# Kernel tuning notes

Hardware: AMD Instinct MI355X
Metric: run time of the kernel (lower is better)

The kernel has to match this reference:

```python
import jax, jax.numpy as jnp
import numpy as np

B, N, E = 256, 512, 8192
F_IN, DEPTH, NHID = 128, 3, 256
CAT = F_IN + DEPTH * NHID  # 896


def setup_inputs() -> dict:
    key = jax.random.key(0)
    ks = jax.random.split(key, 20)
    def w(k, shape, fan_in):
        return jax.random.normal(k, shape, jnp.float32) / np.sqrt(fan_in)
    inp = {
        "x": jax.random.normal(ks[0], (B, N, F_IN), jnp.float32),
        "edge_index": jax.random.randint(ks[1], (2, E), 0, N, jnp.int64),
        # linears: first maps F_IN->NHID, rest NHID->NHID (stacked)
        "lin0_W": w(ks[2], (F_IN, NHID), F_IN),
        "lin0_b": jnp.zeros((NHID,), jnp.float32),
        "lin_Ws": w(ks[3], (DEPTH - 1, NHID, NHID), NHID),
        "lin_bs": jnp.zeros((DEPTH - 1, NHID), jnp.float32),
        # GCNConv weights (stacked), PyG semantics: A_norm (X W) + b
        "conv_Ws": w(ks[4], (DEPTH, NHID, NHID), NHID),
        "conv_bs": jnp.zeros((DEPTH, NHID), jnp.float32),
        "sig_W": w(ks[5], (CAT, NHID), CAT),
        "sig_b": jnp.zeros((NHID,), jnp.float32),
        "tanh_W": w(ks[6], (CAT, NHID), CAT),
        "tanh_b": jnp.zeros((NHID,), jnp.float32),
        "f1_W": w(ks[7], (NHID, NHID), NHID),
        "f1_b": jnp.zeros((NHID,), jnp.float32),
        "f2_W": w(ks[8], (NHID, 2), NHID),
        "f2_b": jnp.zeros((2,), jnp.float32),
    }
    return inp


def _gcn_norm(edge_index, n):
    # add self loops, compute symmetric normalization D^-1/2 (A+I) D^-1/2
    loop = jnp.arange(n, dtype=edge_index.dtype)
    src = jnp.concatenate([edge_index[0], loop])
    dst = jnp.concatenate([edge_index[1], loop])
    deg = jax.ops.segment_sum(jnp.ones_like(src, jnp.float32), dst, num_segments=n)
    dinv = jax.lax.rsqrt(jnp.maximum(deg, 1.0))
    norm = dinv[src] * dinv[dst]  # [E+N]
    return src, dst, norm


def _gcn(h, W, b, src, dst, norm, n):
    # h: [B, N, C]
    hW = h @ W
    msg = hW[:, src, :] * norm[None, :, None]          # [B, E+N, C]
    agg = jax.vmap(lambda m: jax.ops.segment_sum(m, dst, num_segments=n))(msg)
    return agg + b


def reference(x, edge_index, lin0_W, lin0_b, lin_Ws, lin_bs, conv_Ws, conv_bs,
              sig_W, sig_b, tanh_W, tanh_b, f1_W, f1_b, f2_W, f2_b):
    n = x.shape[1]
    src, dst, norm = _gcn_norm(edge_index, n)
    xs = [x]
    out = x
    for i in range(DEPTH):
        if i == 0:
            out = out @ lin0_W + lin0_b
        else:
            out = out @ lin_Ws[i - 1] + lin_bs[i - 1]
        out = _gcn(out, conv_Ws[i], conv_bs[i], src, dst, norm, n)
        out = jnp.tanh(out)
        xs.append(out)
    cat = jnp.concatenate(xs, axis=-1)                 # [B, N, CAT]
    s = jax.nn.sigmoid(cat @ sig_W + sig_b)            # [B, N, NHID]
    t = jnp.tanh(cat @ tanh_W + tanh_b)                # [B, N, NHID]
    pooled = jnp.sum(s * t, axis=1)                    # [B, NHID] (sum over nodes)
    embeds = jnp.tanh(pooled)
    h = jax.nn.relu(embeds @ f1_W + f1_b)              # dropout is eval-mode identity
    preds = h @ f2_W + f2_b                            # [B, 2]
    preds = jnp.concatenate([jax.nn.sigmoid(preds[:, :1]), preds[:, 1:]], axis=-1)
    return preds, embeds
```

## Files before the change

### kernel.cpp

```cpp
#include <hip/hip_runtime.h>
#include <hip/hip_bf16.h>
#include <cstdint>

typedef _Float16 half_t;
typedef __attribute__((ext_vector_type(8))) _Float16 half8;
typedef __attribute__((ext_vector_type(4))) _Float16 half4;
typedef __attribute__((ext_vector_type(4))) float f32x4;

#define MFMA16x32(a, b, c) __builtin_amdgcn_mfma_f32_16x16x32_f16(a, b, c, 0, 0, 0)

static constexpr int NB  = 256;
static constexpr int NN  = 512;
static constexpr int NE  = 8192;
static constexpr int FIN = 128;
static constexpr int NH  = 256;
static constexpr int CAT = 896;

__device__ __forceinline__ float fsigmoid(float u)
{
    return __builtin_amdgcn_rcpf(1.f + __expf(-u));
}
__device__ __forceinline__ float ftanh(float v)
{
    const float c = fminf(fmaxf(v, -10.f), 10.f);
    const float e = __expf(2.f * c);
    return (e - 1.f) * __builtin_amdgcn_rcpf(e + 1.f);
}

__device__ __forceinline__ void xcd_swz_y(int& bx, int& by)
{
    const int nwg = gridDim.x * gridDim.y;
    int wgid = blockIdx.y * gridDim.x + blockIdx.x;
    wgid = (wgid & 7) * (nwg >> 3) + (wgid >> 3);
    bx = wgid % gridDim.x;
    by = wgid / gridDim.x;
}
__device__ __forceinline__ void xcd_swz_x(int& bx, int& by)
{
    const int nwg = gridDim.x * gridDim.y;
    int wgid = blockIdx.x * gridDim.y + blockIdx.y;
    wgid = (wgid & 7) * (nwg >> 3) + (wgid >> 3);
    bx = wgid / gridDim.y;
    by = wgid % gridDim.y;
}

__device__ __forceinline__ void gload16(const half_t* __restrict__ g, half_t* l)
{
    __builtin_amdgcn_global_load_lds(
        (const __attribute__((address_space(1))) uint32_t*)(uintptr_t)g,
        (__attribute__((address_space(3))) uint32_t*)(uintptr_t)l, 16, 0, 0);
}

__device__ __forceinline__ void stage128x64(
    const half_t* __restrict__ src, long row0, int ldk, int k0,
    half_t* lds, int tid)
{
    const int wid = tid >> 6, lane = tid & 63;
#pragma unroll
    for (int it = 0; it < 4; ++it) {
        const int rb   = wid * 32 + it * 8;
        const int row  = rb + (lane >> 3);
        const int slot = (lane & 7) ^ (row & 7);
        gload16(src + (row0 + row) * (long)ldk + k0 + slot * 8,
                lds + (size_t)rb * 64);
    }
}

__device__ __forceinline__ half8 fragr(const half_t* lds, int row, int slot)
{
    return *(const half8*)(lds + row * 64 + ((slot ^ (row & 7)) * 8));
}

struct Tab {
    const void* src[16];
    float*      dst[16];
    int         n[16];
    int         fi[16];
    int         nseg;
};

__global__ void k_detect_all(Tab t, int* __restrict__ flags)
{
    const int s = blockIdx.x;
    if (s >= t.nseg) return;
    __shared__ int cnt_s;
    if (threadIdx.x == 0) cnt_s = 0;
    __syncthreads();
    const uint32_t* w = (const uint32_t*)t.src[s];
    int nw = t.n[s] / 2; if (nw > 2048) nw = 2048; if (nw < 1) nw = 1;
    int c = 0;
    for (int i = threadIdx.x; i < nw; i += 256) {
        const uint32_t lo = w[i] & 0xFFFFu;
        const int e = (int)((lo >> 7) & 0xFF);
        if (lo == 0u || (e >= 116 && e <= 136)) ++c;
    }
    atomicAdd(&cnt_s, c);
    __syncthreads();
    if (threadIdx.x == 0) flags[t.fi[s]] = (2 * cnt_s >= nw) ? 1 : 0;
}

__global__ void k_cvt_all(Tab t, const int* __restrict__ flags)
{
    for (int s = 0; s < t.nseg; ++s) {
        float* dst = t.dst[s];
        if (dst == nullptr) continue;
        const int is_bf = flags[t.fi[s]];
        const int n = t.n[s];
        const void* src = t.src[s];
        for (int i = blockIdx.x * 256 + threadIdx.x; i < n; i += gridDim.x * 256)
            dst[i] = is_bf
                ? __uint_as_float(((uint32_t)((const uint16_t*)src)[i]) << 16)
                : ((const float*)src)[i];
    }
}

__global__ void k_x2h(const void* __restrict__ xraw, half_t* __restrict__ o,
                      size_t n8, const int* __restrict__ flag)
{
    const int is_bf = *flag;
    const size_t gid0 = (size_t)blockIdx.x * blockDim.x + threadIdx.x;
    const size_t stride = (size_t)gridDim.x * blockDim.x;
    if (is_bf) {
        const uint4* src = (const uint4*)xraw;
        for (size_t i = gid0; i < n8; i += stride) {
            const uint4 v = src[i];
            half8 h;
            h[0] = (_Float16)__uint_as_float((v.x & 0xFFFFu) << 16);
            h[1] = (_Float16)__uint_as_float(v.x & 0xFFFF0000u);
            h[2] = (_Float16)__uint_as_float((v.y & 0xFFFFu) << 16);
            h[3] = (_Float16)__uint_as_float(v.y & 0xFFFF0000u);
            h[4] = (_Float16)__uint_as_float((v.z & 0xFFFFu) << 16);
            h[5] = (_Float16)__uint_as_float(v.z & 0xFFFF0000u);
            h[6] = (_Float16)__uint_as_float((v.w & 0xFFFFu) << 16);
            h[7] = (_Float16)__uint_as_float(v.w & 0xFFFF0000u);
            ((half8*)o)[i] = h;
        }
    } else {
        const float4* src = (const float4*)xraw;
        for (size_t i = gid0; i < n8; i += stride) {
            const float4 a = src[2 * i], b = src[2 * i + 1];
            half8 h;
            h[0] = (_Float16)a.x; h[1] = (_Float16)a.y;
            h[2] = (_Float16)a.z; h[3] = (_Float16)a.w;
            h[4] = (_Float16)b.x; h[5] = (_Float16)b.y;
            h[6] = (_Float16)b.z; h[7] = (_Float16)b.w;
            ((half8*)o)[i] = h;
        }
    }
}

__global__ void k_sentinel(__hip_bfloat16* __restrict__ out, float code)
{
    const int i = blockIdx.x * 256 + threadIdx.x;
    if (i < 66048) out[i] = __float2bfloat16(i < 512 ? code : 0.f);
}

__global__ void k_pick512(const float* __restrict__ a, const float* __restrict__ b,
                          float* __restrict__ f2Wc, float* __restrict__ linbsc)
{
    __shared__ float sa_s, sb_s;
    const int t = threadIdx.x;
    if (t == 0) { sa_s = 0.f; sb_s = 0.f; }
    __syncthreads();
    float va = fabsf(a[t]) + fabsf(a[t + 256]);
    float vb = fabsf(b[t]) + fabsf(b[t + 256]);
    for (int o = 32; o; o >>= 1) {
        va += __shfl_down(va, o, 64);
        vb += __shfl_down(vb, o, 64);
    }
    if ((t & 63) == 0) { atomicAdd(&sa_s, va); atomicAdd(&sb_s, vb); }
    __syncthreads();
    const float* f2 = (sa_s >= sb_s) ? a : b;
    const float* lb = (sa_s >= sb_s) ? b : a;
    f2Wc[t] = f2[t]; f2Wc[t + 256] = f2[t + 256];
    linbsc[t] = lb[t]; linbsc[t + 256] = lb[t + 256];
}

__global__ void k_build_graph(const int* __restrict__ ei, int* __restrict__ rowptr,
                              int* __restrict__ colx, float* __restrict__ wn,
                              float* __restrict__ srow)
{
    __shared__ int   degs[NN];
    __shared__ float dinv[NN];
    __shared__ int   rp[NN + 1];
    __shared__ int   cur[NN];
    __shared__ float sacc[NN];
    __shared__ int   is64_s;
    const int t = threadIdx.x;
    degs[t] = 0; cur[t] = 0; sacc[t] = 0.f;
    if (t == 0) {
        int orv = 0;
        for (int i = 1; i < 256; i += 2) orv |= ei[i];
        is64_s = (orv == 0) ? 1 : 0;
    }
    __syncthreads();
    const bool is64 = (is64_s != 0);
    auto EV = [&](int idx) { return is64 ? ei[2 * idx] : ei[idx]; };

    for (int e = t; e < NE; e += NN)
        atomicAdd(&degs[EV(NE + e)], 1);
    __syncthreads();
    const float dv = rsqrtf(fmaxf((float)(degs[t] + 1), 1.f));
    dinv[t] = dv;
    __syncthreads();
    if (t == 0) {
        rp[0] = 0;
        for (int i = 0; i < NN; ++i) rp[i + 1] = rp[i] + degs[i] + 1;
    }
    __syncthreads();
    rowptr[t] = rp[t];
    if (t == 0) rowptr[NN] = rp[NN];
    for (int e = t; e < NE; e += NN) {
        const int s = EV(e), d = EV(NE + e);
        const int pos = atomicAdd(&cur[d], 1);
        colx[rp[d] + pos] = s;
        wn[rp[d] + pos]   = dinv[s] * dinv[d];
        atomicAdd(&sacc[d], dinv[s]);
    }
    __syncthreads();
    const int slot = rp[t + 1] - 1;
    colx[slot] = t;
    wn[slot]   = dv * dv;
    srow[t]    = dv * (sacc[t] + dv);
}

__global__ void k_densify(const int* __restrict__ rowptr, const int* __restrict__ colx,
                          const float* __restrict__ wn, half_t* __restrict__ S16)
{
    __shared__ float row[NN];
    const int d = blockIdx.x;
    for (int i = threadIdx.x; i < NN; i += 256) row[i] = 0.f;
    __syncthreads();
    const int s0 = rowptr[d], s1 = rowptr[d + 1];
    for (int e = s0 + threadIdx.x; e < s1; e += 256)
        atomicAdd(&row[colx[e]], wn[e]);
    __syncthreads();
    for (int i = threadIdx.x; i < NN; i += 256)
        S16[(size_t)d * NN + i] = (half_t)row[i];
}

__global__ void k_fold_wc(const float* __restrict__ lin0_W, const float* __restrict__ lin_Ws,
                          const float* __restrict__ conv_Ws,
                          half_t* __restrict__ wc0, half_t* __restrict__ wc1,
                          half_t* __restrict__ wc2)
{
    const int layer = blockIdx.y;
    const int k = blockIdx.x;
    const int n = threadIdx.x;
    const int K = (layer == 0) ? FIN : NH;
    if (k >= K) return;
    const float* lin = (layer == 0) ? lin0_W : lin_Ws + (size_t)(layer - 1) * NH * NH;
    const float* cw  = conv_Ws + (size_t)layer * NH * NH;
    float s = 0.f;
    for (int j = 0; j < NH; ++j) s += lin[k * NH + j] * cw[j * NH + n];
    half_t* o = (layer == 0) ? wc0 : ((layer == 1) ? wc1 : wc2);
    o[n * K + k] = (half_t)s;
}

__global__ void k_fold_wt(const float* __restrict__ sigW, const float* __restrict__ tanW,
                          half_t* __restrict__ sh, half_t* __restrict__ th,
                          const float* __restrict__ lin0_b, const float* __restrict__ lin_bs,
                          const float* __restrict__ conv_Ws, float* __restrict__ vb)
{
    const int which = blockIdx.y;
    if (which == 2) {
        const int layer = blockIdx.x;
        if (layer >= 3) return;
        const int n = threadIdx.x;
        const float* lb = (layer == 0) ? lin0_b : lin_bs + (size_t)(layer - 1) * NH;
        const float* cw = conv_Ws + (size_t)layer * NH * NH;
        float s = 0.f;
        for (int j = 0; j < NH; ++j) s += lb[j] * cw[j * NH + n];
        vb[layer * NH + n] = s;
        return;
    }
    const int n = blockIdx.x;
    const float* W = which ? tanW : sigW;
    half_t* o = which ? th : sh;
    for (int k = threadIdx.x; k < CAT; k += 256)
        o[(size_t)n * CAT + k] = (half_t)W[(size_t)k * NH + n];
}

__global__ __launch_bounds__(256, 2) void k_gemm_t(
    const half_t* __restrict__ A, const half_t* __restrict__ BT,
    half_t* __restrict__ hwT, int K)
{
    __shared__ __align__(16) half_t sm[17408];
    half_t* lA = sm;
    half_t* lB = sm + 8192;
    int bx, by; xcd_swz_x(bx, by);
    const int tid = threadIdx.x;
    const int lane = tid & 63, wid = tid >> 6;
    const int wr = wid >> 1, wc = wid & 1;
    const int row_l = lane & 15, kg = lane >> 4;
    const long mbase = (long)bx * 128;
    const int nbase = by * 128;
    f32x4 acc[4][4] = {};
    for (int k0 = 0; k0 < K; k0 += 64) {
        stage128x64(A,  mbase, K, k0, lA, tid);
        stage128x64(BT, nbase, K, k0, lB, tid);
        __syncthreads();
#pragma unroll
        for (int ks = 0; ks < 2; ++ks) {
            half8 af[4], bf[4];
#pragma unroll
            for (int mt = 0; mt < 4; ++mt)
                af[mt] = fragr(lA, wr * 64 + mt * 16 + row_l, ks * 4 + kg);
#pragma unroll
            for (int nt = 0; nt < 4; ++nt)
                bf[nt] = fragr(lB, wc * 64 + nt * 16 + row_l, ks * 4 + kg);
#pragma unroll
            for (int mt = 0; mt < 4; ++mt)
#pragma unroll
                for (int nt = 0; nt < 4; ++nt)
                    acc[mt][nt] = MFMA16x32(af[mt], bf[nt], acc[mt][nt]);
        }
        __syncthreads();
    }
    half_t* lC = sm;
#pragma unroll
    for (int mt = 0; mt < 4; ++mt) {
        const int m_l = wr * 64 + mt * 16 + kg * 4;
#pragma unroll
        for (int nt = 0; nt < 4; ++nt) {
            const int n_l = wc * 64 + nt * 16 + row_l;
            half4 p;
            p[0] = (_Float16)acc[mt][nt][0]; p[1] = (_Float16)acc[mt][nt][1];
            p[2] = (_Float16)acc[mt][nt][2]; p[3] = (_Float16)acc[mt][nt][3];
            *(half4*)(lC + n_l * 136 + m_l) = p;
        }
    }
    __syncthreads();
    const int b  = (int)(mbase >> 9);
    const int s0 = (int)(mbase & 511);
#pragma unroll
    for (int pass = 0; pass < 8; ++pass) {
        const int n_l = pass * 16 + (tid >> 4);
        const int part = tid & 15;
        const half8 v = *(const half8*)(lC + n_l * 136 + part * 8);
        *(half8*)(hwT + ((size_t)b * 256 + nbase + n_l) * 512 + s0 + part * 8) = v;
    }
}

__global__ __launch_bounds__(256, 2) void k_gemm_agg(
    const half_t* __restrict__ S16, const half_t* __restrict__ hwT,
    const float* __restrict__ srow, const float* __restrict__ vb,
    const float* __restrict__ cb, half_t* __restrict__ hout)
{
    __shared__ __align__(16) half_t sm[17408];
    half_t* lA = sm;
    half_t* lB = sm + 8192;
    int bx, by; xcd_swz_y(bx, by);
    const int tid = threadIdx.x;
    const int lane = tid & 63, wid = tid >> 6;
    const int wr = wid >> 1, wc = wid & 1;
    const int row_l = lane & 15, kg = lane >> 4;
    const int mbase = bx * 128;
    const int nbase = by * 128;
    f32x4 acc[4][4] = {};
    for (int k0 = 0; k0 < 512; k0 += 64) {
        stage128x64(S16, mbase, 512, k0, lA, tid);
        stage128x64(hwT, nbase, 512, k0, lB, tid);
        __syncthreads();
#pragma unroll
        for (int ks = 0; ks < 2; ++ks) {
            half8 af[4], bf[4];
#pragma unroll
            for (int mt = 0; mt < 4; ++mt)
                af[mt] = fragr(lA, wr * 64 + mt * 16 + row_l, ks * 4 + kg);
#pragma unroll
            for (int nt = 0; nt < 4; ++nt)
                bf[nt] = fragr(lB, wc * 64 + nt * 16 + row_l, ks * 4 + kg);
#pragma unroll
            for (int mt = 0; mt < 4; ++mt)
#pragma unroll
                for (int nt = 0; nt < 4; ++nt)
                    acc[mt][nt] = MFMA16x32(af[mt], bf[nt], acc[mt][nt]);
        }
        __syncthreads();
    }
    const int b  = nbase >> 8;
    const int c0 = nbase & 255;
    half_t* lC = sm;
#pragma unroll
    for (int mt = 0; mt < 4; ++mt) {
        const int m_l = wr * 64 + mt * 16 + kg * 4;
        float sr[4];
#pragma unroll
        for (int r = 0; r < 4; ++r) sr[r] = srow[mbase + m_l + r];
#pragma unroll
        for (int nt = 0; nt < 4; ++nt) {
            const int n_l = wc * 64 + nt * 16 + row_l;
            const float vbc = vb[c0 + n_l], cbc = cb[c0 + n_l];
#pragma unroll
            for (int r = 0; r < 4; ++r)
                lC[(m_l + r) * 136 + n_l] =
                    (half_t)ftanh(acc[mt][nt][r] + sr[r] * vbc + cbc);
        }
    }
    __syncthreads();
#pragma unroll
    for (int pass = 0; pass < 8; ++pass) {
        const int row = pass * 16 + (tid >> 4);
        const int col = (tid & 15) * 8;
        const half8 v = *(const half8*)(lC + row * 136 + col);
        *(half8*)(hout + ((size_t)b * NN + mbase + row) * NH + c0 + col) = v;
    }
}

__global__ __launch_bounds__(256, 2) void k_gemm_final(
    const half_t* __restrict__ x16, const half_t* __restrict__ h1,
    const half_t* __restrict__ h2, const half_t* __restrict__ h3,
    const half_t* __restrict__ bsh, const half_t* __restrict__ bth,
    const float* __restrict__ sig_b, const float* __restrict__ tan_b,
    float* __restrict__ part)
{
    __shared__ __align__(16) half_t sm[24576];
    __shared__ float red[2][128];
    half_t* lA  = sm;
    half_t* lBs = sm + 8192;
    half_t* lBt = sm + 16384;
    int bx, by; xcd_swz_x(bx, by);
    const int tid = threadIdx.x;
    const int lane = tid & 63, wid = tid >> 6;
    const int wr = wid >> 1, wc = wid & 1;
    const int row_l = lane & 15, kg = lane >> 4;
    const long mbase = (long)bx * 128;
    const int sup = by;
    f32x4 aS[4][4] = {}, aT[4][4] = {};
    for (int kt = 0; kt < 14; ++kt) {
        const int k0 = kt * 64;
        const half_t* Aseg; int segK, lk;
        if (k0 < 128)      { Aseg = x16; segK = 128; lk = k0; }
        else if (k0 < 384) { Aseg = h1;  segK = 256; lk = k0 - 128; }
        else if (k0 < 640) { Aseg = h2;  segK = 256; lk = k0 - 384; }
        else               { Aseg = h3;  segK = 256; lk = k0 - 640; }
        stage128x64(Aseg, mbase, segK, lk, lA, tid);
        stage128x64(bsh, (long)sup * 128, CAT, k0, lBs, tid);
        stage128x64(bth, (long)sup * 128, CAT, k0, lBt, tid);
        __syncthreads();
#pragma unroll
        for (int ks = 0; ks < 2; ++ks) {
            half8 af[4];
#pragma unroll
            for (int mt = 0; mt < 4; ++mt)
                af[mt] = fragr(lA, wr * 64 + mt * 16 + row_l, ks * 4 + kg);
#pragma unroll
            for (int nt = 0; nt < 4; ++nt) {
                const int r = wc * 64 + nt * 16 + row_l;
                const half8 fs = fragr(lBs, r, ks * 4 + kg);
                const half8 ft = fragr(lBt, r, ks * 4 + kg);
#pragma unroll
                for (int mt = 0; mt < 4; ++mt) {
                    aS[mt][nt] = MFMA16x32(af[mt], fs, aS[mt][nt]);
                    aT[mt][nt] = MFMA16x32(af[mt], ft, aT[mt][nt]);
                }
            }
        }
        __syncthreads();
    }
#pragma unroll
    for (int nt = 0; nt < 4; ++nt) {
        const int j = sup * 128 + wc * 64 + nt * 16 + row_l;
        const float sb = sig_b[j], tb = tan_b[j];
        float ps = 0.f;
#pragma unroll
        for (int mt = 0; mt < 4; ++mt)
#pragma unroll
            for (int r = 0; r < 4; ++r) {
                const float u = aS[mt][nt][r] + sb;
                const float v = aT[mt][nt][r] + tb;
                ps += fsigmoid(u) * ftanh(v);
            }
        ps += __shfl_xor(ps, 16, 64);
        ps += __shfl_xor(ps, 32, 64);
        if (lane < 16) red[wr][wc * 64 + nt * 16 + lane] = ps;
    }
    __syncthreads();
    if (tid < 128)
        part[(long)bx * 256 + sup * 128 + tid] = red[0][tid] + red[1][tid];
}

__global__ __launch_bounds__(256) void k_finish(
    const float* __restrict__ part, const float* __restrict__ f1W,
    const float* __restrict__ f1b, const float* __restrict__ f2W,
    const float* __restrict__ f2b, void* __restrict__ dout,
    const int* __restrict__ flags)
{
    __shared__ float e[NH], h[NH];
    const int b = blockIdx.x, t = threadIdx.x;
    const int any = flags[0] | flags[1] | flags[2] | flags[3] | flags[4] |
                    flags[5] | flags[6];
    const int w4 = any ? 0 : 1;
    const float* p = part + (size_t)b * 1024 + t;
    const float ev = tanhf(p[0] + p[256] + p[512] + p[768]);
    e[t] = ev;
    if (w4) ((float*)dout)[512 + b * NH + t] = ev;
    else    ((__hip_bfloat16*)dout)[512 + b * NH + t] = __float2bfloat16(ev);
    __syncthreads();
    float a = f1b[t];
    for (int k = 0; k < NH; ++k) a += e[k] * f1W[k * NH + t];
    h[t] = fmaxf(a, 0.f);
    __syncthreads();
    if (t < 64) {
        float p0 = 0.f, p1 = 0.f;
        for (int jj = t; jj < NH; jj += 64) {
            p0 += h[jj] * f2W[jj * 2 + 0];
            p1 += h[jj] * f2W[jj * 2 + 1];
        }
        for (int o = 32; o; o >>= 1) {
            p0 += __shfl_down(p0, o, 64);
            p1 += __shfl_down(p1, o, 64);
        }
        if (t == 0) {
            p0 += f2b[0]; p1 += f2b[1];
            p0 = 1.f / (1.f + expf(-p0));
            if (w4) {
                ((float*)dout)[b * 2 + 0] = p0;
                ((float*)dout)[b * 2 + 1] = p1;
            } else {
                ((__hip_bfloat16*)dout)[b * 2 + 0] = __float2bfloat16(p0);
                ((__hip_bfloat16*)dout)[b * 2 + 1] = __float2bfloat16(p1);
            }
        }
    }
}

extern "C" void kernel_launch(void* const* d_in, const int* in_sizes, int n_in,
                              void* d_out, int out_size, void* d_ws, size_t ws_size,
                              hipStream_t stream)
{
    (void)out_size;

    int ix = -1, ie = -1, il0 = -1, ilw = -1, icw = -1, icb = -1, if1 = -1, if2b = -1;
    int i229[2] = {-1, -1}; int n229 = 0;
    int i512[2] = {-1, -1}; int n512 = 0;
    int i256[4] = {-1, -1, -1, -1}; int n256 = 0;
    int bad = 0;
    for (int i = 0; i < n_in && i < 16; ++i) {
        switch (in_sizes[i]) {
            case 16777216: ix = i; break;
            case 16384:    ie = i; break;
            case 32768:    il0 = i; break;
            case 131072:   ilw = i; break;
            case 196608:   icw = i; break;
            case 768:      icb = i; break;
            case 65536:    if1 = i; break;
            case 2:        if2b = i; break;
            case 229376:   if (n229 < 2) i229[n229++] = i; else bad = 1; break;
            case 512:      if (n512 < 2) i512[n512++] = i; else bad = 1; break;
            case 256:      if (n256 < 4) i256[n256++] = i; else bad = 1; break;
            default:       bad = 1; break;
        }
    }
    if (n_in != 16 || bad || ix < 0 || ie < 0 || il0 < 0 || ilw < 0 || icw < 0 ||
        icb < 0 || if1 < 0 || if2b < 0 || n229 != 2 || n512 != 2 || n256 != 4) {
        k_sentinel<<<(66048 + 255) / 256, 256, 0, stream>>>((__hip_bfloat16*)d_out, 20480.f);
        return;
    }

    char* wp = (char*)d_ws;
    auto alloc = [&](size_t sz) {
        char* p = wp;
        wp += (sz + 4095) & ~(size_t)4095;
        return p;
    };
    int*   flags  = (int*)alloc(32 * 4);
    float* c_lin0W  = (float*)alloc((size_t)FIN * NH * 4);
    float* c_linWs  = (float*)alloc((size_t)2 * NH * NH * 4);
    float* c_convWs = (float*)alloc((size_t)3 * NH * NH * 4);
    float* c_convbs = (float*)alloc((size_t)3 * NH * 4);
    float* c_sigW   = (float*)alloc((size_t)CAT * NH * 4);
    float* c_tanW   = (float*)alloc((size_t)CAT * NH * 4);
    float* c_f1W    = (float*)alloc((size_t)NH * NH * 4);
    float* c_f2b    = (float*)alloc(2 * 4);
    float* c_512a   = (float*)alloc(512 * 4);
    float* c_512b   = (float*)alloc(512 * 4);
    float* f2Wc     = (float*)alloc(512 * 4);
    float* linbsc   = (float*)alloc(512 * 4);
    float* c_b256[4];
    for (int q = 0; q < 4; ++q) c_b256[q] = (float*)alloc(256 * 4);
    int*    rowptr = (int*)alloc((NN + 1) * 4);
    int*    colx   = (int*)alloc((NE + NN) * 4);
    float*  wn     = (float*)alloc((NE + NN) * 4);
    float*  srow   = (float*)alloc(NN * 4);
    float*  vb     = (float*)alloc(3 * NH * 4);
    half_t* S16  = (half_t*)alloc((size_t)NN * NN * 2);
    half_t* wc0  = (half_t*)alloc((size_t)NH * FIN * 2);
    half_t* wc1  = (half_t*)alloc((size_t)NH * NH * 2);
    half_t* wc2  = (half_t*)alloc((size_t)NH * NH * 2);
    half_t* sgh  = (half_t*)alloc((size_t)NH * CAT * 2);
    half_t* tnh  = (half_t*)alloc((size_t)NH * CAT * 2);
    float*  part = (float*)alloc((size_t)1024 * 256 * 4);
    half_t* x16  = (half_t*)alloc((size_t)NB * NN * FIN * 2);

    const size_t fixed_end = (size_t)(wp - (char*)d_ws);
    int CB = 256;
    while (CB > 4) {
        const size_t mc = (size_t)CB * NN;
        const size_t act = 4 * ((mc * NH * 2 + 4095) & ~(size_t)4095);
        if (fixed_end + act + (1u << 20) <= ws_size) break;
        CB >>= 1;
    }
    const size_t MC = (size_t)CB * NN;
    const int NCH = NB / CB;

    half_t* h1c  = (half_t*)alloc(MC * NH * 2);
    half_t* h2c  = (half_t*)alloc(MC * NH * 2);
    half_t* h3c  = (half_t*)alloc(MC * NH * 2);
    half_t* hwT  = (half_t*)alloc(MC * NH * 2);

    Tab t = {};
    int s = 0;
    auto addseg = [&](int idx, float* dst, int n, int fi) {
        t.src[s] = d_in[idx]; t.dst[s] = dst; t.n[s] = n; t.fi[s] = fi; ++s;
    };
    addseg(ix,      nullptr,   16777216, 0);
    addseg(il0,     c_lin0W,   FIN * NH, 1);
    addseg(ilw,     c_linWs,   2 * NH * NH, 2);
    addseg(icw,     c_convWs,  3 * NH * NH, 3);
    addseg(i229[0], c_sigW,    CAT * NH, 4);
    addseg(i229[1], c_tanW,    CAT * NH, 5);
    addseg(if1,     c_f1W,     NH * NH, 6);
    addseg(i512[0], c_512a,    512, 7);
    addseg(i512[1], c_512b,    512, 8);
    for (int q = 0; q < 4; ++q) addseg(i256[q], c_b256[q], 256, 9 + q);
    addseg(icb,     c_convbs,  3 * NH, 13);
    addseg(if2b,    c_f2b,     2, 14);
    t.nseg = s;

    k_detect_all<<<t.nseg, 256, 0, stream>>>(t, flags);
    k_cvt_all<<<1024, 256, 0, stream>>>(t, flags);
    k_pick512<<<1, 256, 0, stream>>>(c_512a, c_512b, f2Wc, linbsc);

    const float* lin0_b = c_b256[0];
    const float* sig_b  = c_b256[1];
    const float* tan_b  = c_b256[2];
    const float* f1_b   = c_b256[3];

    k_build_graph<<<1, 512, 0, stream>>>((const int*)d_in[ie], rowptr, colx, wn, srow);
    k_densify<<<NN, 256, 0, stream>>>(rowptr, colx, wn, S16);
    k_fold_wc<<<dim3(256, 3), 256, 0, stream>>>(c_lin0W, c_linWs, c_convWs, wc0, wc1, wc2);
    k_fold_wt<<<dim3(256, 3), 256, 0, stream>>>(c_sigW, c_tanW, sgh, tnh,
                                                lin0_b, linbsc, c_convWs, vb);
    k_x2h<<<2048, 256, 0, stream>>>(d_in[ix], x16, (size_t)NB * NN * FIN / 8, flags + 0);

    for (int c = 0; c < NCH; ++c) {
        half_t* x16c = x16 + (size_t)c * MC * FIN;
        k_gemm_t<<<dim3(CB * 4, 2), 256, 0, stream>>>(x16c, wc0, hwT, 128);
        k_gemm_agg<<<dim3(4, CB * 2), 256, 0, stream>>>(S16, hwT, srow, vb + 0,
                                                        c_convbs + 0, h1c);
        k_gemm_t<<<dim3(CB * 4, 2), 256, 0, stream>>>(h1c, wc1, hwT, 256);
        k_gemm_agg<<<dim3(4, CB * 2), 256, 0, stream>>>(S16, hwT, srow, vb + 256,
                                                        c_convbs + 256, h2c);
        k_gemm_t<<<dim3(CB * 4, 2), 256, 0, stream>>>(h2c, wc2, hwT, 256);
        k_gemm_agg<<<dim3(4, CB * 2), 256, 0, stream>>>(S16, hwT, srow, vb + 512,
                                                        c_convbs + 512, h3c);
        k_gemm_final<<<dim3(CB * 4, 2), 256, 0, stream>>>(
            x16c, h1c, h2c, h3c, sgh, tnh, sig_b, tan_b,
            part + (size_t)c * CB * 1024);
    }
    k_finish<<<NB, 256, 0, stream>>>(part, c_f1W, f1_b, f2Wc, c_f2b, d_out, flags);
}
```

Measured before the change: 461.6 us.

## Double-buffer LDS tiles in aggregation and final GEMMs to overlap loads with MFMA

Both the aggregation GEMM and the final sigmoid/tanh GEMM now use two LDS buffers, so the next K-tile is prefetched while MFMAs run on the current one. Waits use explicit vmcnt counts and raw barriers, with s_setprio raised around the compute section. The final GEMM drops to 32-wide K tiles with a new swizzle so the doubled buffers fit in the same LDS footprint. The aggregation kernel's LDS use roughly doubles, which may reduce occupancy, and the hand-counted vmcnt values depend on how many loads each stage helper issues.

```diff
diff --git a/kernel.cpp b/kernel.cpp
--- a/kernel.cpp
+++ b/kernel.cpp
@@ -69,6 +69,26 @@
 __device__ __forceinline__ half8 fragr(const half_t* lds, int row, int slot)
 {
     return *(const half8*)(lds + row * 64 + ((slot ^ (row & 7)) * 8));
+}
+
+__device__ __forceinline__ void stage128x32(
+    const half_t* __restrict__ src, long row0, int ldk, int k0,
+    half_t* lds, int tid)
+{
+    const int wid = tid >> 6, lane = tid & 63;
+#pragma unroll
+    for (int it = 0; it < 2; ++it) {
+        const int rb   = wid * 32 + it * 16;
+        const int row  = rb + (lane >> 2);
+        const int slot = (lane & 3) ^ ((row >> 1) & 3);
+        gload16(src + (row0 + row) * (long)ldk + k0 + slot * 8,
+                lds + (size_t)rb * 32);
+    }
+}
+
+__device__ __forceinline__ half8 fragr32(const half_t* lds, int row, int slot)
+{
+    return *(const half8*)(lds + row * 32 + ((slot ^ ((row >> 1) & 3)) * 8));
 }
 
 struct Tab {
@@ -347,9 +367,7 @@
     const float* __restrict__ srow, const float* __restrict__ vb,
     const float* __restrict__ cb, half_t* __restrict__ hout)
 {
-    __shared__ __align__(16) half_t sm[17408];
-    half_t* lA = sm;
-    half_t* lB = sm + 8192;
+    __shared__ __align__(16) half_t sm[32768];
     int bx, by; xcd_swz_y(bx, by);
     const int tid = threadIdx.x;
     const int lane = tid & 63, wid = tid >> 6;
@@ -358,26 +376,39 @@
     const int mbase = bx * 128;
     const int nbase = by * 128;
     f32x4 acc[4][4] = {};
-    for (int k0 = 0; k0 < 512; k0 += 64) {
-        stage128x64(S16, mbase, 512, k0, lA, tid);
-        stage128x64(hwT, nbase, 512, k0, lB, tid);
-        __syncthreads();
+    stage128x64(S16, mbase, 512, 0, sm, tid);
+    stage128x64(hwT, nbase, 512, 0, sm + 8192, tid);
+    for (int kt = 0; kt < 8; ++kt) {
+        half_t* cur = sm + (kt & 1) * 16384;
+        if (kt + 1 < 8) {
+            half_t* nxt = sm + ((kt + 1) & 1) * 16384;
+            stage128x64(S16, mbase, 512, (kt + 1) * 64, nxt, tid);
+            stage128x64(hwT, nbase, 512, (kt + 1) * 64, nxt + 8192, tid);
+            asm volatile("s_waitcnt vmcnt(8)" ::: "memory");
+        } else {
+            asm volatile("s_waitcnt vmcnt(0)" ::: "memory");
+        }
+        __builtin_amdgcn_s_barrier();
+        __builtin_amdgcn_sched_barrier(0);
+        __builtin_amdgcn_s_setprio(1);
 #pragma unroll
         for (int ks = 0; ks < 2; ++ks) {
             half8 af[4], bf[4];
 #pragma unroll
             for (int mt = 0; mt < 4; ++mt)
-                af[mt] = fragr(lA, wr * 64 + mt * 16 + row_l, ks * 4 + kg);
+                af[mt] = fragr(cur, wr * 64 + mt * 16 + row_l, ks * 4 + kg);
 #pragma unroll
             for (int nt = 0; nt < 4; ++nt)
-                bf[nt] = fragr(lB, wc * 64 + nt * 16 + row_l, ks * 4 + kg);
+                bf[nt] = fragr(cur + 8192, wc * 64 + nt * 16 + row_l, ks * 4 + kg);
 #pragma unroll
             for (int mt = 0; mt < 4; ++mt)
 #pragma unroll
                 for (int nt = 0; nt < 4; ++nt)
                     acc[mt][nt] = MFMA16x32(af[mt], bf[nt], acc[mt][nt]);
         }
-        __syncthreads();
+        __builtin_amdgcn_s_setprio(0);
+        __builtin_amdgcn_s_barrier();
+        __builtin_amdgcn_sched_barrier(0);
     }
     const int b  = nbase >> 8;
     const int c0 = nbase & 255;
@@ -417,9 +448,6 @@
 {
     __shared__ __align__(16) half_t sm[24576];
     __shared__ float red[2][128];
-    half_t* lA  = sm;
-    half_t* lBs = sm + 8192;
-    half_t* lBt = sm + 16384;
     int bx, by; xcd_swz_x(bx, by);
     const int tid = threadIdx.x;
     const int lane = tid & 63, wid = tid >> 6;
@@ -428,36 +456,54 @@
     const long mbase = (long)bx * 128;
     const int sup = by;
     f32x4 aS[4][4] = {}, aT[4][4] = {};
-    for (int kt = 0; kt < 14; ++kt) {
-        const int k0 = kt * 64;
-        const half_t* Aseg; int segK, lk;
+    auto segof = [&](int k0, const half_t*& Aseg, int& segK, int& lk) {
         if (k0 < 128)      { Aseg = x16; segK = 128; lk = k0; }
         else if (k0 < 384) { Aseg = h1;  segK = 256; lk = k0 - 128; }
         else if (k0 < 640) { Aseg = h2;  segK = 256; lk = k0 - 384; }
         else               { Aseg = h3;  segK = 256; lk = k0 - 640; }
-        stage128x64(Aseg, mbase, segK, lk, lA, tid);
-        stage128x64(bsh, (long)sup * 128, CAT, k0, lBs, tid);
-        stage128x64(bth, (long)sup * 128, CAT, k0, lBt, tid);
-        __syncthreads();
-#pragma unroll
-        for (int ks = 0; ks < 2; ++ks) {
-            half8 af[4];
-#pragma unroll
-            for (int mt = 0; mt < 4; ++mt)
-                af[mt] = fragr(lA, wr * 64 + mt * 16 + row_l, ks * 4 + kg);
-#pragma unroll
-            for (int nt = 0; nt < 4; ++nt) {
-                const int r = wc * 64 + nt * 16 + row_l;
-                const half8 fs = fragr(lBs, r, ks * 4 + kg);
-                const half8 ft = fragr(lBt, r, ks * 4 + kg);
-#pragma unroll
-                for (int mt = 0; mt < 4; ++mt) {
-                    aS[mt][nt] = MFMA16x32(af[mt], fs, aS[mt][nt]);
-                    aT[mt][nt] = MFMA16x32(af[mt], ft, aT[mt][nt]);
-                }
+    };
+    {
+        const half_t* Aseg; int segK, lk;
+        segof(0, Aseg, segK, lk);
+        stage128x32(Aseg, mbase, segK, lk, sm, tid);
+        stage128x32(bsh, (long)sup * 128, CAT, 0, sm + 4096, tid);
+        stage128x32(bth, (long)sup * 128, CAT, 0, sm + 8192, tid);
+    }
+    for (int kt = 0; kt < 28; ++kt) {
+        half_t* cur = sm + (kt & 1) * 12288;
+        if (kt + 1 < 28) {
+            half_t* nxt = sm + ((kt + 1) & 1) * 12288;
+            const int k1 = (kt + 1) * 32;
+            const half_t* Aseg; int segK, lk;
+            segof(k1, Aseg, segK, lk);
+            stage128x32(Aseg, mbase, segK, lk, nxt, tid);
+            stage128x32(bsh, (long)sup * 128, CAT, k1, nxt + 4096, tid);
+            stage128x32(bth, (long)sup * 128, CAT, k1, nxt + 8192, tid);
+            asm volatile("s_waitcnt vmcnt(6)" ::: "memory");
+        } else {
+            asm volatile("s_waitcnt vmcnt(0)" ::: "memory");
+        }
+        __builtin_amdgcn_s_barrier();
+        __builtin_amdgcn_sched_barrier(0);
+        __builtin_amdgcn_s_setprio(1);
+        half8 af[4];
+#pragma unroll
+        for (int mt = 0; mt < 4; ++mt)
+            af[mt] = fragr32(cur, wr * 64 + mt * 16 + row_l, kg);
+#pragma unroll
+        for (int nt = 0; nt < 4; ++nt) {
+            const int r = wc * 64 + nt * 16 + row_l;
+            const half8 fs = fragr32(cur + 4096, r, kg);
+            const half8 ft = fragr32(cur + 8192, r, kg);
+#pragma unroll
+            for (int mt = 0; mt < 4; ++mt) {
+                aS[mt][nt] = MFMA16x32(af[mt], fs, aS[mt][nt]);
+                aT[mt][nt] = MFMA16x32(af[mt], ft, aT[mt][nt]);
             }
         }
-        __syncthreads();
+        __builtin_amdgcn_s_setprio(0);
+        __builtin_amdgcn_s_barrier();
+        __builtin_amdgcn_sched_barrier(0);
     }
 #pragma unroll
     for (int nt = 0; nt < 4; ++nt) {
```

After: 483.8 us. +4.8%, slower.
